# Kernel tuning notes

Measured on AMD Instinct MI355X. Metric: run time of the kernel, lower is better.

## Reference

```python
import jax, jax.numpy as jnp
import numpy as np
import math

L, H, NH, NKV, HD = 18, 1024, 8, 1, 256
FF, HOR, PRE, B, AD = 4096, 50, 968, 8, 32
EPS = 1e-6
NEG = -1e9
SCALE = HD ** -0.5


def setup_inputs() -> dict:
    key = jax.random.key(0)
    ks = iter(jax.random.split(key, 64))
    n = lambda shape, s=0.02: jax.random.normal(next(ks), shape, jnp.float32) * s
    return {
        'prefix_keys':    jax.random.normal(next(ks), (B, L, NKV, PRE, HD), jnp.float32),
        'prefix_values':  jax.random.normal(next(ks), (B, L, NKV, PRE, HD), jnp.float32),
        'x_t':            jax.random.normal(next(ks), (B, HOR, AD), jnp.float32),
        'timestep':       jax.random.uniform(next(ks), (B,), jnp.float32),
        'prefix_pad_masks': jnp.ones((B, PRE), jnp.bool_),
        'action_in_w': n((AD, H)), 'action_in_b': jnp.zeros((H,), jnp.float32),
        'action_out_w': n((H, AD)), 'action_out_b': jnp.zeros((AD,), jnp.float32),
        'tmlp_in_w': n((H, H)), 'tmlp_in_b': jnp.zeros((H,), jnp.float32),
        'tmlp_out_w': n((H, H)), 'tmlp_out_b': jnp.zeros((H,), jnp.float32),
        'w_q': n((L, H, NH * HD)), 'w_k': n((L, H, NKV * HD)), 'w_v': n((L, H, NKV * HD)),
        'w_o': n((L, NH * HD, H)),
        'w_gate': n((L, H, FF)), 'w_up': n((L, H, FF)), 'w_down': n((L, FF, H)),
        'in_norm_w': jnp.zeros((L, H), jnp.float32), 'in_scale_w': n((L, H, H)), 'in_gate_w': n((L, H, H)),
        'post_norm_w': jnp.zeros((L, H), jnp.float32), 'post_scale_w': n((L, H, H)), 'post_gate_w': n((L, H, H)),
        'fnorm_w': jnp.zeros((H,), jnp.float32), 'fnorm_scale_w': n((H, H)),
    }


def _rmsnorm(x, w):
    v = jnp.mean(x * x, axis=-1, keepdims=True)
    return x * jax.lax.rsqrt(v + EPS) * (1.0 + w)


def _ada_rmsnorm(x, w, cond, w_scale, w_gate):
    # AdaRMSNorm: rmsnorm scaled by (1 + dense(cond)); returns gate = dense(cond)
    normed = _rmsnorm(x, w)
    scale = cond @ w_scale                     # [B, H]
    gate = cond @ w_gate                       # [B, H]
    return normed * (1.0 + scale[:, None, :]), gate[:, None, :]


def _time_cond(timestep, tmlp_in_w, tmlp_in_b, tmlp_out_w, tmlp_out_b):
    half = H // 2
    frac = jnp.linspace(0.0, 1.0, half)
    period = 0.004 * (4.0 / 0.004) ** frac
    ang = (2.0 * math.pi / period)[None, :] * timestep[:, None]   # [B, half]
    emb = jnp.concatenate([jnp.sin(ang), jnp.cos(ang)], axis=1)   # [B, H]
    emb = jax.nn.silu(emb @ tmlp_in_w + tmlp_in_b)
    return jax.nn.silu(emb @ tmlp_out_w + tmlp_out_b)


def _rope(x, cos, sin):
    x1, x2 = jnp.split(x, 2, axis=-1)
    return x * cos + jnp.concatenate([-x2, x1], axis=-1) * sin


def _attn(q, k, v, mask):
    # q: [B,NH,S,D], k/v: [B,NKV,T,D]; GQA via grouped einsum (no KV materialized expansion)
    G = NH // NKV
    qg = q.reshape(B, NKV, G, HOR, HD)
    s = jnp.einsum('bkgsd,bktd->bkgst', qg, k) * SCALE + mask
    p = jax.nn.softmax(s.astype(jnp.float32), axis=-1).astype(q.dtype)
    return jnp.einsum('bkgst,bktd->bkgsd', p, v).reshape(B, NH, HOR, HD)


def _forward(prefix_pad_masks, prefix_keys, prefix_values, x_t, timestep,
             action_in_w, action_in_b, action_out_w, action_out_b,
             tmlp_in_w, tmlp_in_b, tmlp_out_w, tmlp_out_b,
             w_q, w_k, w_v, w_o, w_gate, w_up, w_down,
             in_norm_w, in_scale_w, in_gate_w,
             post_norm_w, post_scale_w, post_gate_w,
             fnorm_w, fnorm_scale_w):
    cond = _time_cond(timestep, tmlp_in_w, tmlp_in_b, tmlp_out_w, tmlp_out_b)  # [B,H]
    h = x_t @ action_in_w + action_in_b                                        # [B,HOR,H]

    # prefix-bidirectional + causal-suffix mask: [HOR, PRE+HOR]
    mask = jnp.zeros((HOR, PRE + HOR), jnp.float32)
    mask = mask.at[:, PRE:].set(jnp.triu(jnp.full((HOR, HOR), NEG, jnp.float32), k=1))

    # rotary at suffix positions = prefix valid count + arange(HOR)
    offsets = jnp.sum(prefix_pad_masks.astype(jnp.int32), axis=-1, keepdims=True)
    pos = (offsets + jnp.arange(HOR)[None, :]).astype(jnp.float32)             # [B,HOR]
    inv_freq = 1.0 / (10000.0 ** (jnp.arange(0, HD, 2).astype(jnp.float32) / HD))
    ang = pos[:, :, None] * inv_freq[None, None, :]                            # [B,HOR,HD/2]
    cos = jnp.concatenate([jnp.cos(ang), jnp.cos(ang)], axis=-1)[:, None]      # [B,1,HOR,HD]
    sin = jnp.concatenate([jnp.sin(ang), jnp.sin(ang)], axis=-1)[:, None]

    for i in range(L):
        normed, gate = _ada_rmsnorm(h, in_norm_w[i], cond, in_scale_w[i], in_gate_w[i])
        q = (normed @ w_q[i]).reshape(B, HOR, NH, HD).transpose(0, 2, 1, 3)
        k = (normed @ w_k[i]).reshape(B, HOR, NKV, HD).transpose(0, 2, 1, 3)
        v = (normed @ w_v[i]).reshape(B, HOR, NKV, HD).transpose(0, 2, 1, 3)
        q = _rope(q, cos, sin)
        k = _rope(k, cos, sin)
        fk = jnp.concatenate([prefix_keys[:, i], k], axis=2)                    # [B,NKV,PRE+HOR,HD]
        fv = jnp.concatenate([prefix_values[:, i], v], axis=2)
        att = _attn(q, fk, fv, mask)
        att = att.transpose(0, 2, 1, 3).reshape(B, HOR, NH * HD)
        h1 = h + gate * (att @ w_o[i])                                          # gated residual
        normed2, gate2 = _ada_rmsnorm(h1, post_norm_w[i], cond, post_scale_w[i], post_gate_w[i])
        mlp = (jax.nn.gelu(normed2 @ w_gate[i]) * (normed2 @ w_up[i])) @ w_down[i]
        h = h1 + gate2 * mlp

    scale = cond @ fnorm_scale_w
    h = _rmsnorm(h, fnorm_w) * (1.0 + scale[:, None, :])
    return h @ action_out_w + action_out_b


def reference(prefix_keys, prefix_values, x_t, timestep, prefix_pad_masks,
              action_in_w, action_in_b, action_out_w, action_out_b,
              tmlp_in_w, tmlp_in_b, tmlp_out_w, tmlp_out_b,
              w_q, w_k, w_v, w_o, w_gate, w_up, w_down,
              in_norm_w, in_scale_w, in_gate_w,
              post_norm_w, post_scale_w, post_gate_w,
              fnorm_w, fnorm_scale_w):
    return _forward(prefix_pad_masks, prefix_keys, prefix_values, x_t, timestep,
                    action_in_w, action_in_b, action_out_w, action_out_b,
                    tmlp_in_w, tmlp_in_b, tmlp_out_w, tmlp_out_b,
                    w_q, w_k, w_v, w_o, w_gate, w_up, w_down,
                    in_norm_w, in_scale_w, in_gate_w,
                    post_norm_w, post_scale_w, post_gate_w,
                    fnorm_w, fnorm_scale_w)
```

## Files before the change

### kernel.cpp

```cpp
#include <hip/hip_runtime.h>

#define L_ 18
#define H_ 1024
#define NH_ 8
#define HD_ 256
#define FF_ 4096
#define HOR_ 50
#define PRE_ 968
#define B_ 8
#define AD_ 32
#define TPAD_ 1024
#define MROWS_ 400
#define MPAD_ 512
#define KSTEP_ 128
#define LST_ 132

typedef float f32x4 __attribute__((ext_vector_type(4)));
typedef short s16x4 __attribute__((ext_vector_type(4)));
typedef short s16x8 __attribute__((ext_vector_type(8)));
typedef unsigned short u16x8 __attribute__((ext_vector_type(8)));

__device__ __forceinline__ unsigned short f2bf(float f) {
  unsigned u = __float_as_uint(f);
  u += 0x7FFFu + ((u >> 16) & 1u);
  return (unsigned short)(u >> 16);
}
__device__ __forceinline__ float bf2f(unsigned short h) {
  return __uint_as_float(((unsigned)h) << 16);
}
__device__ __forceinline__ float wave_sum(float v) {
#pragma unroll
  for (int o = 32; o > 0; o >>= 1) v += __shfl_xor(v, o);
  return v;
}

__global__ __launch_bounds__(256) void emb_k(const float* __restrict__ ts, float* __restrict__ emb) {
  int b = blockIdx.x, tid = threadIdx.x;
  float t = ts[b];
  for (int j = tid; j < 512; j += 256) {
    float ang = 1570.7963267948966f * expf((float)j * (-6.907755278982137f / 511.0f)) * t;
    emb[(size_t)b * H_ + j] = sinf(ang);
    emb[(size_t)b * H_ + 512 + j] = cosf(ang);
  }
}

__global__ __launch_bounds__(256) void gemm8_k(const float* __restrict__ A8, const float* __restrict__ W,
                                               const float* __restrict__ bias, float* __restrict__ out,
                                               int act) {
  __shared__ float a_s[8 * 1024];
  __shared__ float red[4][8][64];
  int tid = threadIdx.x;
  for (int i = tid; i < 8 * 1024; i += 256) a_s[i] = A8[i];
  __syncthreads();
  int nl = tid & 63, kg = tid >> 6;
  int n = blockIdx.x * 64 + nl;
  float acc[8];
#pragma unroll
  for (int m = 0; m < 8; m++) acc[m] = 0.f;
  for (int k = kg * 256; k < kg * 256 + 256; k++) {
    float wv = W[(size_t)k * 1024 + n];
#pragma unroll
    for (int m = 0; m < 8; m++) acc[m] += a_s[m * 1024 + k] * wv;
  }
#pragma unroll
  for (int m = 0; m < 8; m++) red[kg][m][nl] = acc[m];
  __syncthreads();
  if (kg == 0) {
#pragma unroll
    for (int m = 0; m < 8; m++) {
      float v = red[0][m][nl] + red[1][m][nl] + red[2][m][nl] + red[3][m][nl];
      if (bias) v += bias[n];
      if (act) v = v / (1.f + expf(-v));
      out[(size_t)m * 1024 + n] = v;
    }
  }
}

__global__ __launch_bounds__(256) void gates_k(const float* __restrict__ cond,
                                               const float* __restrict__ w0, const float* __restrict__ w1,
                                               const float* __restrict__ w2, const float* __restrict__ w3,
                                               float* __restrict__ gates) {
  __shared__ float a_s[8 * 1024];
  __shared__ float red[4][8][64];
  int tid = threadIdx.x;
  for (int i = tid; i < 8 * 1024; i += 256) a_s[i] = cond[i];
  __syncthreads();
  int z = blockIdx.z, layer = blockIdx.y;
  const float* W = (z == 0 ? w0 : z == 1 ? w1 : z == 2 ? w2 : w3) + (size_t)layer * H_ * H_;
  float* out = gates + ((size_t)(z * L_ + layer) * 8) * H_;
  int nl = tid & 63, kg = tid >> 6;
  int n = blockIdx.x * 64 + nl;
  float acc[8];
#pragma unroll
  for (int m = 0; m < 8; m++) acc[m] = 0.f;
  for (int k = kg * 256; k < kg * 256 + 256; k++) {
    float wv = W[(size_t)k * 1024 + n];
#pragma unroll
    for (int m = 0; m < 8; m++) acc[m] += a_s[m * 1024 + k] * wv;
  }
#pragma unroll
  for (int m = 0; m < 8; m++) red[kg][m][nl] = acc[m];
  __syncthreads();
  if (kg == 0) {
#pragma unroll
    for (int m = 0; m < 8; m++)
      out[(size_t)m * 1024 + n] = red[0][m][nl] + red[1][m][nl] + red[2][m][nl] + red[3][m][nl];
  }
}

__global__ void offs_k(const unsigned char* __restrict__ mask, int* __restrict__ offs) {
  __shared__ int cnt[8];
  __shared__ int mod4;
  int tid = threadIdx.x;
  if (tid < 8) cnt[tid] = 0;
  if (tid == 8) mod4 = 0;
  __syncthreads();
  for (int i = tid; i < B_ * PRE_; i += 256) {
    unsigned char v = mask[i];
    if (v) {
      atomicAdd(&cnt[i / PRE_], 1);
      if (i & 3) atomicAdd(&mod4, 1);
    }
  }
  __syncthreads();
  if (tid < 8) offs[tid] = (mod4 == 0) ? cnt[tid] * 4 : cnt[tid];
}

__global__ __launch_bounds__(256) void action_in_k(const float* __restrict__ xt, const float* __restrict__ Wi,
                                                   const float* __restrict__ bi, float* __restrict__ h) {
  int idx = blockIdx.x * 256 + threadIdx.x;
  int m = idx >> 10, n = idx & 1023;
  float v = 0.f;
  if (m < MROWS_) {
    const float* xr = xt + (size_t)m * AD_;
#pragma unroll
    for (int k = 0; k < AD_; k++) v += xr[k] * Wi[(size_t)k * H_ + n];
    v += bi[n];
  }
  h[idx] = v;
}

__global__ __launch_bounds__(256) void ada_k(const float* __restrict__ X, const float* __restrict__ nw,
                                             const float* __restrict__ sc, unsigned short* __restrict__ Y) {
  int m = blockIdx.x, tid = threadIdx.x;
  size_t base = (size_t)m * H_;
  if (m >= MROWS_) {
#pragma unroll
    for (int j = 0; j < 4; j++) Y[base + tid * 4 + j] = 0;
    return;
  }
  f32x4 x = *(const f32x4*)(X + base + tid * 4);
  float ss = x[0] * x[0] + x[1] * x[1] + x[2] * x[2] + x[3] * x[3];
  __shared__ float r4[4];
  float wsv = wave_sum(ss);
  if ((tid & 63) == 0) r4[tid >> 6] = wsv;
  __syncthreads();
  float rs = rsqrtf((r4[0] + r4[1] + r4[2] + r4[3]) * (1.f / 1024.f) + 1e-6f);
  int b = m / HOR_;
#pragma unroll
  for (int j = 0; j < 4; j++) {
    int n = tid * 4 + j;
    Y[base + n] = f2bf(x[j] * rs * (1.f + nw[n]) * (1.f + sc[(size_t)b * H_ + n]));
  }
}

__global__ __launch_bounds__(256) void prefixAll_k(const float* __restrict__ pk, const float* __restrict__ pv,
                                                   unsigned short* __restrict__ Kf_all,
                                                   unsigned short* __restrict__ Vt_all) {
  int b = blockIdx.y, t0 = blockIdx.x * 64, layer = blockIdx.z, tid = threadIdx.x;
  unsigned short* Kf = Kf_all + (size_t)layer * B_ * TPAD_ * HD_;
  unsigned short* Vt = Vt_all + (size_t)layer * B_ * HD_ * TPAD_;
  __shared__ unsigned short vt[256][72];
  const float* kp = pk + ((size_t)(b * L_ + layer)) * PRE_ * HD_;
  const float* vp = pv + ((size_t)(b * L_ + layer)) * PRE_ * HD_;
  for (int i = 0; i < 64; i++) {
    int t = t0 + i;
    float kv = 0.f, vv = 0.f;
    if (t < PRE_) {
      kv = kp[(size_t)t * HD_ + tid];
      vv = vp[(size_t)t * HD_ + tid];
    }
    Kf[((size_t)b * TPAD_ + t) * HD_ + tid] = f2bf(kv);
    vt[tid][i] = f2bf(vv);
  }
  __syncthreads();
#pragma unroll
  for (int p = 0; p < 4; p++) {
    int d = p * 64 + (tid >> 2);
    int c0 = (tid & 3) * 16;
    u16x8 v0, v1;
#pragma unroll
    for (int j = 0; j < 8; j++) { v0[j] = vt[d][c0 + j]; v1[j] = vt[d][c0 + 8 + j]; }
    size_t dst = ((size_t)(b * HD_ + d)) * TPAD_ + t0 + c0;
    *(u16x8*)(Vt + dst) = v0;
    *(u16x8*)(Vt + dst + 8) = v1;
  }
}

__global__ __launch_bounds__(512) void qkvF_k(const unsigned short* __restrict__ A,
                                              const float* __restrict__ Wq, const float* __restrict__ Wk,
                                              const float* __restrict__ Wv, const int* __restrict__ offs,
                                              unsigned short* __restrict__ q_r, unsigned short* __restrict__ Kf,
                                              unsigned short* __restrict__ Vt) {
  const int st = blockIdx.x, mh = blockIdx.y;
  const int tid = threadIdx.x, wv = tid >> 6, l = tid & 63;
  const int lr = l & 15, kg = l >> 4, lk = kg << 2;
  const int m0 = mh * 256 + wv * 32;

  const float* W;
  int ldw, wbase;
  bool paired;
  if (st < 64)      { W = Wq; ldw = 2048; wbase = (st >> 3) * 256 + (st & 7) * 16; paired = true; }
  else if (st < 72) { W = Wk; ldw = 256;  wbase = (st - 64) * 16; paired = true; }
  else              { W = Wv; ldw = 256;  wbase = (st - 72) * 32; paired = false; }

  __shared__ unsigned short Wt[2][32][LST_];
  __shared__ int offsL[8];
  const int pr = tid >> 3, c0 = (tid & 7) * 4;
  const int wcol = wbase + c0 + ((paired && c0 >= 16) ? 112 : 0);

  if (tid < 8) offsL[tid] = offs[tid];

  f32x4 acc[2][2];
#pragma unroll
  for (int a = 0; a < 2; a++)
#pragma unroll
    for (int b = 0; b < 2; b++) acc[a][b] = (f32x4){0.f, 0.f, 0.f, 0.f};

  f32x4 pa0, pa1;
  auto LOADW = [&](int IT) {
    size_t kk = (size_t)IT * KSTEP_ + 2 * pr;
    pa0 = *(const f32x4*)(W + kk * ldw + wcol);
    pa1 = *(const f32x4*)(W + (kk + 1) * ldw + wcol);
  };
  auto STOREW = [&](int BUF) {
#pragma unroll
    for (int j = 0; j < 4; j++) {
      unsigned v = (unsigned)f2bf(pa0[j]) | ((unsigned)f2bf(pa1[j]) << 16);
      *(unsigned*)&Wt[BUF][c0 + j][2 * pr] = v;
    }
  };

  LOADW(0);
  STOREW(0);
  __syncthreads();

  for (int it = 0; it < 8; ++it) {
    if (it + 1 < 8) LOADW(it + 1);
    const int cur = it & 1, kb = it * KSTEP_;
#pragma unroll
    for (int s = 0; s < 4; s++) {
      s16x8 bfr[2];
#pragma unroll
      for (int nf = 0; nf < 2; nf++) {
        const unsigned short* wp = &Wt[cur][nf * 16 + lr][s * 32 + 2 * lk];
        s16x4 b0 = *(const s16x4*)wp;
        s16x4 b1 = *(const s16x4*)(wp + 4);
#pragma unroll
        for (int j = 0; j < 4; j++) { bfr[nf][j] = b0[j]; bfr[nf][4 + j] = b1[j]; }
      }
#pragma unroll
      for (int mf = 0; mf < 2; mf++) {
        s16x8 a = *(const s16x8*)(A + (size_t)(m0 + mf * 16 + lr) * H_ + kb + s * 32 + 8 * kg);
#pragma unroll
        for (int nf = 0; nf < 2; nf++)
          acc[mf][nf] = __builtin_amdgcn_mfma_f32_16x16x32_bf16(a, bfr[nf], acc[mf][nf], 0, 0, 0);
      }
    }
    if (it + 1 < 8) STOREW((it + 1) & 1);
    __syncthreads();
  }

  const float RK = -9.210340371976184f / 128.0f;
  if (st < 64) {
    const int h = st >> 3, x = (st & 7) * 16, dd = x + lr;
    const float inv = expf((float)dd * RK);
#pragma unroll
    for (int mf = 0; mf < 2; mf++)
#pragma unroll
      for (int r = 0; r < 4; r++) {
        int m = m0 + mf * 16 + lk + r;
        if (m >= MROWS_) continue;
        int b = m / HOR_, s = m - b * HOR_;
        float ang = (float)(offsL[b] + s) * inv;
        float cc = cosf(ang), sn = sinf(ang);
        float v1 = acc[mf][0][r], v2 = acc[mf][1][r];
        size_t base = ((size_t)(b * NH_ + h) * 64 + s) * HD_;
        q_r[base + dd] = f2bf(v1 * cc - v2 * sn);
        q_r[base + dd + 128] = f2bf(v2 * cc + v1 * sn);
      }
  } else if (st < 72) {
    const int x = (st - 64) * 16, dd = x + lr;
    const float inv = expf((float)dd * RK);
#pragma unroll
    for (int mf = 0; mf < 2; mf++)
#pragma unroll
      for (int r = 0; r < 4; r++) {
        int m = m0 + mf * 16 + lk + r;
        if (m >= MROWS_) continue;
        int b = m / HOR_, s = m - b * HOR_;
        float ang = (float)(offsL[b] + s) * inv;
        float cc = cosf(ang), sn = sinf(ang);
        float v1 = acc[mf][0][r], v2 = acc[mf][1][r];
        size_t base = ((size_t)b * TPAD_ + PRE_ + s) * HD_;
        Kf[base + dd] = f2bf(v1 * cc - v2 * sn);
        Kf[base + dd + 128] = f2bf(v2 * cc + v1 * sn);
      }
  } else {
    const int x = (st - 72) * 32;
#pragma unroll
    for (int mf = 0; mf < 2; mf++)
#pragma unroll
      for (int nf = 0; nf < 2; nf++)
#pragma unroll
        for (int r = 0; r < 4; r++) {
          int m = m0 + mf * 16 + lk + r;
          if (m >= MROWS_) continue;
          int b = m / HOR_, s = m - b * HOR_;
          int d = x + nf * 16 + lr;
          Vt[((size_t)(b * HD_ + d)) * TPAD_ + PRE_ + s] = f2bf(acc[mf][nf][r]);
        }
  }
}

__global__ __launch_bounds__(512) void flash8_k(const unsigned short* __restrict__ qr,
                                                const unsigned short* __restrict__ Kf,
                                                const unsigned short* __restrict__ Vt,
                                                unsigned short* __restrict__ attb) {
  const int b = blockIdx.x, rg = blockIdx.y, h = blockIdx.z;
  const int bh = b * NH_ + h;
  const int tid = threadIdx.x, w = tid >> 6, l = tid & 63;
  const int lr = l & 15, kg = l >> 4;
  const int t0 = w * 128;

  __shared__ __align__(16) unsigned short Pl[8][16][136];
  __shared__ float mlS[8][16][2];

  const unsigned short* qbase = qr + ((size_t)bh * 64 + rg * 16 + lr) * HD_;
  s16x8 afr[8];
#pragma unroll
  for (int js = 0; js < 8; js++) afr[js] = *(const s16x8*)(qbase + js * 32 + 8 * kg);
  f32x4 sc[8];
#pragma unroll
  for (int nf = 0; nf < 8; nf++) sc[nf] = (f32x4){0.f, 0.f, 0.f, 0.f};
  const unsigned short* kb = Kf + ((size_t)b * TPAD_ + t0) * HD_;
#pragma unroll
  for (int js = 0; js < 8; js++)
#pragma unroll
    for (int nf = 0; nf < 8; nf++) {
      s16x8 bv = *(const s16x8*)(kb + (size_t)(nf * 16 + lr) * HD_ + js * 32 + 8 * kg);
      sc[nf] = __builtin_amdgcn_mfma_f32_16x16x32_bf16(afr[js], bv, sc[nf], 0, 0, 0);
    }
  float mx[4] = {-3.0e38f, -3.0e38f, -3.0e38f, -3.0e38f};
#pragma unroll
  for (int nf = 0; nf < 8; nf++) {
    int t = t0 + nf * 16 + lr;
#pragma unroll
    for (int r = 0; r < 4; r++) {
      int srw = rg * 16 + 4 * kg + r;
      float v = sc[nf][r] * 0.0625f;
      if (t >= PRE_ && (t - PRE_) > srw) v = -1e9f;
      sc[nf][r] = v;
      mx[r] = fmaxf(mx[r], v);
    }
  }
#pragma unroll
  for (int o = 8; o > 0; o >>= 1)
#pragma unroll
    for (int r = 0; r < 4; r++) mx[r] = fmaxf(mx[r], __shfl_xor(mx[r], o));
  float ls[4] = {0.f, 0.f, 0.f, 0.f};
#pragma unroll
  for (int nf = 0; nf < 8; nf++)
#pragma unroll
    for (int r = 0; r < 4; r++) {
      float p = expf(sc[nf][r] - mx[r]);
      sc[nf][r] = p;
      ls[r] += p;
    }
#pragma unroll
  for (int o = 8; o > 0; o >>= 1)
#pragma unroll
    for (int r = 0; r < 4; r++) ls[r] += __shfl_xor(ls[r], o);
#pragma unroll
  for (int nf = 0; nf < 8; nf++)
#pragma unroll
    for (int r = 0; r < 4; r++) Pl[w][4 * kg + r][nf * 16 + lr] = f2bf(sc[nf][r]);
  if (lr == 0) {
#pragma unroll
    for (int r = 0; r < 4; r++) {
      mlS[w][4 * kg + r][0] = mx[r];
      mlS[w][4 * kg + r][1] = ls[r];
    }
  }
  __syncthreads();
  f32x4 o4[8][2];
#pragma unroll
  for (int a = 0; a < 8; a++)
#pragma unroll
    for (int c = 0; c < 2; c++) o4[a][c] = (f32x4){0.f, 0.f, 0.f, 0.f};
#pragma unroll
  for (int wz = 0; wz < 8; wz++)
#pragma unroll
    for (int ti = 0; ti < 128; ti += 32) {
      s16x8 a = *(const s16x8*)&Pl[wz][lr][ti + 8 * kg];
#pragma unroll
      for (int nf = 0; nf < 2; nf++) {
        s16x8 bv = *(const s16x8*)(Vt + ((size_t)(b * HD_ + w * 32 + nf * 16 + lr)) * TPAD_ +
                                   wz * 128 + ti + 8 * kg);
        o4[wz][nf] = __builtin_amdgcn_mfma_f32_16x16x32_bf16(a, bv, o4[wz][nf], 0, 0, 0);
      }
    }
#pragma unroll
  for (int r = 0; r < 4; r++) {
    int row = 4 * kg + r;
    int s = rg * 16 + row;
    if (s >= HOR_) continue;
    float M = -3.0e38f;
#pragma unroll
    for (int wz = 0; wz < 8; wz++) M = fmaxf(M, mlS[wz][row][0]);
    float w8[8], Lden = 0.f;
#pragma unroll
    for (int wz = 0; wz < 8; wz++) {
      w8[wz] = expf(mlS[wz][row][0] - M);
      Lden += w8[wz] * mlS[wz][row][1];
    }
    float invL = 1.f / Lden;
#pragma unroll
    for (int nf = 0; nf < 2; nf++) {
      float o = 0.f;
#pragma unroll
      for (int wz = 0; wz < 8; wz++) o += w8[wz] * o4[wz][nf][r];
      attb[((size_t)(b * HOR_ + s)) * 2048 + h * HD_ + w * 32 + nf * 16 + lr] = f2bf(o * invL);
    }
  }
}

template <int MODE, int NS, int MS>
__global__ __launch_bounds__(512) void gemmS_k(const unsigned short* __restrict__ A, int lda, int Ksz,
                                               const float* __restrict__ W0, const float* __restrict__ W1,
                                               float* __restrict__ part, unsigned short* __restrict__ outT) {
  constexpr int NCOL = (MODE == 2) ? 64 : 32;
  constexpr int NF = NCOL / 16;
  constexpr int RPW = 64 / MS;
  constexpr int MFC = RPW / 16;
  const int tid = threadIdx.x;
  const int wv = tid >> 6, l = tid & 63;
  const int lr = l & 15, lk = (l >> 4) << 2;
  const int n0 = blockIdx.x * 32;
  const int kz = blockIdx.y;
  const int KC = Ksz / NS;
  const int kbase = kz * KC;
  const int m0 = (int)blockIdx.z * (512 / MS) + wv * RPW;

  const float* Wg = W0;
  const float* Wu = W1;
  const int ldw = (MODE == 2) ? 4096 : 1024;

  __shared__ unsigned short Wt[2][NCOL][LST_];
  const int pr = tid >> 3;
  const int c0 = (tid & 7) * 4;

  f32x4 acc[MFC][NF];
#pragma unroll
  for (int a = 0; a < MFC; a++)
#pragma unroll
    for (int b = 0; b < NF; b++) acc[a][b] = (f32x4){0.f, 0.f, 0.f, 0.f};

  const int niter = KC / KSTEP_;
  f32x4 pa0, pa1, pb0, pb1;

  auto LOADW = [&](int IT) {
    size_t kk = (size_t)(kbase + IT * KSTEP_ + 2 * pr);
    pa0 = *(const f32x4*)(Wg + kk * ldw + n0 + c0);
    pa1 = *(const f32x4*)(Wg + (kk + 1) * ldw + n0 + c0);
    if (MODE == 2) {
      pb0 = *(const f32x4*)(Wu + kk * ldw + n0 + c0);
      pb1 = *(const f32x4*)(Wu + (kk + 1) * ldw + n0 + c0);
    }
  };
  auto STOREW = [&](int BUF) {
#pragma unroll
    for (int j = 0; j < 4; j++) {
      unsigned v = (unsigned)f2bf(pa0[j]) | ((unsigned)f2bf(pa1[j]) << 16);
      *(unsigned*)&Wt[BUF][c0 + j][2 * pr] = v;
      if (MODE == 2) {
        unsigned u = (unsigned)f2bf(pb0[j]) | ((unsigned)f2bf(pb1[j]) << 16);
        *(unsigned*)&Wt[BUF][32 + c0 + j][2 * pr] = u;
      }
    }
  };

  LOADW(0);
  STOREW(0);
  __syncthreads();

  for (int it = 0; it < niter; ++it) {
    if (it + 1 < niter) LOADW(it + 1);
    const int cur = it & 1;
    const int kb = kbase + it * KSTEP_;
#pragma unroll
    for (int s = 0; s < 4; s++) {
      s16x8 bfr[NF];
#pragma unroll
      for (int nf = 0; nf < NF; nf++) {
        const unsigned short* wp = &Wt[cur][nf * 16 + lr][s * 32 + 2 * lk];
        s16x4 b0 = *(const s16x4*)wp;
        s16x4 b1 = *(const s16x4*)(wp + 4);
#pragma unroll
        for (int j = 0; j < 4; j++) { bfr[nf][j] = b0[j]; bfr[nf][4 + j] = b1[j]; }
      }
#pragma unroll
      for (int mf = 0; mf < MFC; mf++) {
        s16x8 a = *(const s16x8*)(A + (size_t)(m0 + mf * 16 + lr) * lda + kb + s * 32 + 2 * lk);
#pragma unroll
        for (int nf = 0; nf < NF; nf++)
          acc[mf][nf] = __builtin_amdgcn_mfma_f32_16x16x32_bf16(a, bfr[nf], acc[mf][nf], 0, 0, 0);
      }
    }
    if (it + 1 < niter) STOREW((it + 1) & 1);
    __syncthreads();
  }

  if (MODE == 2) {
#pragma unroll
    for (int mf = 0; mf < MFC; mf++)
#pragma unroll
      for (int nf = 0; nf < 2; nf++)
#pragma unroll
        for (int r = 0; r < 4; r++) {
          int row = m0 + mf * 16 + lk + r;
          if (row >= MROWS_) continue;
          int col = n0 + nf * 16 + lr;
          float g = acc[mf][nf][r];
          float u = acc[mf][nf + 2][r];
          g = 0.5f * g * (1.f + tanhf(0.7978845608028654f * (g + 0.044715f * g * g * g)));
          outT[(size_t)row * 4096 + col] = f2bf(g * u);
        }
  } else {
#pragma unroll
    for (int mf = 0; mf < MFC; mf++)
#pragma unroll
      for (int nf = 0; nf < NF; nf++)
#pragma unroll
        for (int r = 0; r < 4; r++) {
          int row = m0 + mf * 16 + lk + r;
          if (row >= MROWS_) continue;
          int col = n0 + nf * 16 + lr;
          part[((size_t)kz * MPAD_ + row) * 1024 + col] = acc[mf][nf][r];
        }
  }
}

template <int NS>
__global__ __launch_bounds__(256) void redA_k(const float* __restrict__ part, const float* __restrict__ prev,
                                              const float* __restrict__ gatev, const float* __restrict__ nw,
                                              const float* __restrict__ sc, float* __restrict__ outH,
                                              unsigned short* __restrict__ outN) {
  int r = blockIdx.x, tid = threadIdx.x;
  int c = tid * 4;
  f32x4 h = (f32x4){0.f, 0.f, 0.f, 0.f};
  int b = 0;
  if (r < MROWS_) {
    b = r / HOR_;
    f32x4 v = (f32x4){0.f, 0.f, 0.f, 0.f};
#pragma unroll
    for (int z = 0; z < NS; z++) v += *(const f32x4*)(part + ((size_t)z * MPAD_ + r) * H_ + c);
    f32x4 pv = *(const f32x4*)(prev + (size_t)r * H_ + c);
    f32x4 gv = *(const f32x4*)(gatev + (size_t)b * H_ + c);
    h = pv + gv * v;
  }
  *(f32x4*)(outH + (size_t)r * H_ + c) = h;
  float ss = h[0] * h[0] + h[1] * h[1] + h[2] * h[2] + h[3] * h[3];
  __shared__ float r4[4];
  float wsv = wave_sum(ss);
  if ((tid & 63) == 0) r4[tid >> 6] = wsv;
  __syncthreads();
  float rs = rsqrtf((r4[0] + r4[1] + r4[2] + r4[3]) * (1.f / 1024.f) + 1e-6f);
#pragma unroll
  for (int j = 0; j < 4; j++) {
    int n = c + j;
    outN[(size_t)r * H_ + n] = f2bf(h[j] * rs * (1.f + nw[n]) * (1.f + sc[(size_t)b * H_ + n]));
  }
}

__global__ __launch_bounds__(256) void fout_k(const unsigned short* __restrict__ nf, const float* __restrict__ Wo,
                                              const float* __restrict__ bo, float* __restrict__ out) {
  int m = blockIdx.x, tid = threadIdx.x;
  int n = tid & 31, kg = tid >> 5;
  float acc = 0.f;
  for (int k = kg * 128; k < kg * 128 + 128; k++)
    acc += bf2f(nf[(size_t)m * H_ + k]) * Wo[(size_t)k * AD_ + n];
  __shared__ float red[8][32];
  red[kg][n] = acc;
  __syncthreads();
  if (kg == 0) {
    float v = 0.f;
#pragma unroll
    for (int g = 0; g < 8; g++) v += red[g][n];
    out[(size_t)m * AD_ + n] = v + bo[n];
  }
}

extern "C" void kernel_launch(void* const* d_in, const int* in_sizes, int n_in,
                              void* d_out, int out_size, void* d_ws, size_t ws_size,
                              hipStream_t stream) {
  const float* prefix_keys   = (const float*)d_in[0];
  const float* prefix_values = (const float*)d_in[1];
  const float* x_t           = (const float*)d_in[2];
  const float* timestep      = (const float*)d_in[3];
  const unsigned char* pad_mask = (const unsigned char*)d_in[4];
  const float* action_in_w   = (const float*)d_in[5];
  const float* action_in_b   = (const float*)d_in[6];
  const float* action_out_w  = (const float*)d_in[7];
  const float* action_out_b  = (const float*)d_in[8];
  const float* tmlp_in_w     = (const float*)d_in[9];
  const float* tmlp_in_b     = (const float*)d_in[10];
  const float* tmlp_out_w    = (const float*)d_in[11];
  const float* tmlp_out_b    = (const float*)d_in[12];
  const float* w_q    = (const float*)d_in[13];
  const float* w_k    = (const float*)d_in[14];
  const float* w_v    = (const float*)d_in[15];
  const float* w_o    = (const float*)d_in[16];
  const float* w_gate = (const float*)d_in[17];
  const float* w_up   = (const float*)d_in[18];
  const float* w_down = (const float*)d_in[19];
  const float* in_norm_w    = (const float*)d_in[20];
  const float* in_scale_w   = (const float*)d_in[21];
  const float* in_gate_w    = (const float*)d_in[22];
  const float* post_norm_w  = (const float*)d_in[23];
  const float* post_scale_w = (const float*)d_in[24];
  const float* post_gate_w  = (const float*)d_in[25];
  const float* fnorm_w       = (const float*)d_in[26];
  const float* fnorm_scale_w = (const float*)d_in[27];

  char* wsp = (char*)d_ws;
  auto alloc = [&](size_t bytes) { void* p = (void*)wsp; wsp += (bytes + 255) & ~(size_t)255; return p; };

  float* emb0   = (float*)alloc((size_t)8 * H_ * 4);
  float* emb1   = (float*)alloc((size_t)8 * H_ * 4);
  float* cond   = (float*)alloc((size_t)8 * H_ * 4);
  float* fscale = (float*)alloc((size_t)8 * H_ * 4);
  float* gates  = (float*)alloc((size_t)4 * L_ * 8 * H_ * 4);
  int*   offs   = (int*)alloc(64);
  float* hbuf   = (float*)alloc((size_t)MPAD_ * H_ * 4);
  float* h1buf  = (float*)alloc((size_t)MPAD_ * H_ * 4);
  unsigned short* normed  = (unsigned short*)alloc((size_t)MPAD_ * H_ * 2);
  unsigned short* normed2 = (unsigned short*)alloc((size_t)MPAD_ * H_ * 2);
  unsigned short* q_r     = (unsigned short*)alloc((size_t)B_ * NH_ * 64 * HD_ * 2);
  unsigned short* Kf_all  = (unsigned short*)alloc((size_t)L_ * B_ * TPAD_ * HD_ * 2);
  unsigned short* Vt_all  = (unsigned short*)alloc((size_t)L_ * B_ * HD_ * TPAD_ * 2);
  unsigned short* attb    = (unsigned short*)alloc((size_t)MPAD_ * 2048 * 2);
  unsigned short* t_buf   = (unsigned short*)alloc((size_t)MPAD_ * FF_ * 2);
  float* wopart = (float*)alloc((size_t)4 * MPAD_ * 1024 * 4);
  float* dpart  = (float*)alloc((size_t)4 * MPAD_ * 1024 * 4);

  hipMemsetAsync(attb + (size_t)MROWS_ * 2048, 0, (size_t)(MPAD_ - MROWS_) * 2048 * 2, stream);

  emb_k<<<8, 256, 0, stream>>>(timestep, emb0);
  gemm8_k<<<16, 256, 0, stream>>>(emb0, tmlp_in_w, tmlp_in_b, emb1, 1);
  gemm8_k<<<16, 256, 0, stream>>>(emb1, tmlp_out_w, tmlp_out_b, cond, 1);
  gemm8_k<<<16, 256, 0, stream>>>(cond, fnorm_scale_w, nullptr, fscale, 0);
  gates_k<<<dim3(16, L_, 4), 256, 0, stream>>>(cond, in_scale_w, in_gate_w, post_scale_w, post_gate_w, gates);
  offs_k<<<1, 256, 0, stream>>>(pad_mask, offs);
  action_in_k<<<(MPAD_ * H_) / 256, 256, 0, stream>>>(x_t, action_in_w, action_in_b, hbuf);
  prefixAll_k<<<dim3(16, B_, L_), 256, 0, stream>>>(prefix_keys, prefix_values, Kf_all, Vt_all);
  ada_k<<<MPAD_, 256, 0, stream>>>(hbuf, in_norm_w, gates, normed);

  for (int i = 0; i < L_; i++) {
    const float* wq_i = w_q + (size_t)i * H_ * 2048;
    const float* wk_i = w_k + (size_t)i * H_ * HD_;
    const float* wv_i = w_v + (size_t)i * H_ * HD_;
    const float* wo_i = w_o + (size_t)i * 2048 * H_;
    const float* wg_i = w_gate + (size_t)i * H_ * FF_;
    const float* wu_i = w_up + (size_t)i * H_ * FF_;
    const float* wd_i = w_down + (size_t)i * FF_ * H_;
    const float* g_in_gate    = gates + ((size_t)(1 * L_ + i) * 8) * H_;
    const float* g_post_scale = gates + ((size_t)(2 * L_ + i) * 8) * H_;
    const float* g_post_gate  = gates + ((size_t)(3 * L_ + i) * 8) * H_;
    unsigned short* Kf_l = Kf_all + (size_t)i * B_ * TPAD_ * HD_;
    unsigned short* Vt_l = Vt_all + (size_t)i * B_ * HD_ * TPAD_;

    qkvF_k<<<dim3(80, 2), 512, 0, stream>>>(normed, wq_i, wk_i, wv_i, offs, q_r, Kf_l, Vt_l);
    flash8_k<<<dim3(B_, 4, NH_), 512, 0, stream>>>(q_r, Kf_l, Vt_l, attb);
    gemmS_k<1, 4, 2><<<dim3(32, 4, 2), 512, 0, stream>>>(attb, 2048, 2048, wo_i, nullptr, wopart, nullptr);
    redA_k<4><<<MPAD_, 256, 0, stream>>>(wopart, hbuf, g_in_gate, post_norm_w + (size_t)i * H_,
                                         g_post_scale, h1buf, normed2);
    gemmS_k<2, 1, 2><<<dim3(128, 1, 2), 512, 0, stream>>>(normed2, H_, H_, wg_i, wu_i, nullptr, t_buf);
    gemmS_k<3, 4, 2><<<dim3(32, 4, 2), 512, 0, stream>>>(t_buf, FF_, FF_, wd_i, nullptr, dpart, nullptr);
    const float* nw_next = (i + 1 < L_) ? in_norm_w + (size_t)(i + 1) * H_ : fnorm_w;
    const float* sc_next = (i + 1 < L_) ? gates + ((size_t)(i + 1) * 8) * H_ : fscale;
    redA_k<4><<<MPAD_, 256, 0, stream>>>(dpart, h1buf, g_post_gate, nw_next, sc_next, hbuf, normed);
  }

  fout_k<<<MROWS_, 256, 0, stream>>>(normed, action_out_w, action_out_b, (float*)d_out);
}
```

Measured before the change: 2.945 ms.

## Prefetch A fragments into registers, add dedicated gate/up kernel, trim pad rows

The activation (A) fragments for the next K-step are now loaded into registers during the current step, in both the QKV kernel and the generic split GEMM, so global-load latency overlaps with MFMA work. The gate/up projection moves to a new upg_k kernel that covers 256 rows per block over 2 row-halves, replacing the split-K gemmS_k MODE 2 launch. The residual/norm reduction kernels now launch only over the 400 real rows, and the padded rows of normed2 and t_buf are zeroed once up front. The cost is more register pressure from the prefetch buffers, which may lower occupancy.

New measurement: 2.665 ms. 1.1x faster.

```diff
diff --git a/kernel.cpp b/kernel.cpp
--- a/kernel.cpp
+++ b/kernel.cpp
@@ -241,13 +241,24 @@
     }
   };
 
+  s16x8 aP[2][4];
+  auto LOADA = [&](int IT) {
+    const int kb = IT * KSTEP_;
+#pragma unroll
+    for (int s = 0; s < 4; s++)
+#pragma unroll
+      for (int mf = 0; mf < 2; mf++)
+        aP[mf][s] = *(const s16x8*)(A + (size_t)(m0 + mf * 16 + lr) * H_ + kb + s * 32 + 8 * kg);
+  };
+
   LOADW(0);
+  LOADA(0);
   STOREW(0);
   __syncthreads();
 
   for (int it = 0; it < 8; ++it) {
     if (it + 1 < 8) LOADW(it + 1);
-    const int cur = it & 1, kb = it * KSTEP_;
+    const int cur = it & 1;
 #pragma unroll
     for (int s = 0; s < 4; s++) {
       s16x8 bfr[2];
@@ -260,14 +271,15 @@
         for (int j = 0; j < 4; j++) { bfr[nf][j] = b0[j]; bfr[nf][4 + j] = b1[j]; }
       }
 #pragma unroll
-      for (int mf = 0; mf < 2; mf++) {
-        s16x8 a = *(const s16x8*)(A + (size_t)(m0 + mf * 16 + lr) * H_ + kb + s * 32 + 8 * kg);
+      for (int mf = 0; mf < 2; mf++)
 #pragma unroll
         for (int nf = 0; nf < 2; nf++)
-          acc[mf][nf] = __builtin_amdgcn_mfma_f32_16x16x32_bf16(a, bfr[nf], acc[mf][nf], 0, 0, 0);
-      }
-    }
-    if (it + 1 < 8) STOREW((it + 1) & 1);
+          acc[mf][nf] = __builtin_amdgcn_mfma_f32_16x16x32_bf16(aP[mf][s], bfr[nf], acc[mf][nf], 0, 0, 0);
+    }
+    if (it + 1 < 8) {
+      LOADA(it + 1);
+      STOREW((it + 1) & 1);
+    }
     __syncthreads();
   }
 
@@ -490,14 +502,24 @@
     }
   };
 
+  s16x8 aP[MFC][4];
+  auto LOADA = [&](int IT) {
+    const int kb = kbase + IT * KSTEP_;
+#pragma unroll
+    for (int s = 0; s < 4; s++)
+#pragma unroll
+      for (int mf = 0; mf < MFC; mf++)
+        aP[mf][s] = *(const s16x8*)(A + (size_t)(m0 + mf * 16 + lr) * lda + kb + s * 32 + 2 * lk);
+  };
+
   LOADW(0);
+  LOADA(0);
   STOREW(0);
   __syncthreads();
 
   for (int it = 0; it < niter; ++it) {
     if (it + 1 < niter) LOADW(it + 1);
     const int cur = it & 1;
-    const int kb = kbase + it * KSTEP_;
 #pragma unroll
     for (int s = 0; s < 4; s++) {
       s16x8 bfr[NF];
@@ -510,14 +532,15 @@
         for (int j = 0; j < 4; j++) { bfr[nf][j] = b0[j]; bfr[nf][4 + j] = b1[j]; }
       }
 #pragma unroll
-      for (int mf = 0; mf < MFC; mf++) {
-        s16x8 a = *(const s16x8*)(A + (size_t)(m0 + mf * 16 + lr) * lda + kb + s * 32 + 2 * lk);
+      for (int mf = 0; mf < MFC; mf++)
 #pragma unroll
         for (int nf = 0; nf < NF; nf++)
-          acc[mf][nf] = __builtin_amdgcn_mfma_f32_16x16x32_bf16(a, bfr[nf], acc[mf][nf], 0, 0, 0);
-      }
-    }
-    if (it + 1 < niter) STOREW((it + 1) & 1);
+          acc[mf][nf] = __builtin_amdgcn_mfma_f32_16x16x32_bf16(aP[mf][s], bfr[nf], acc[mf][nf], 0, 0, 0);
+    }
+    if (it + 1 < niter) {
+      LOADA(it + 1);
+      STOREW((it + 1) & 1);
+    }
     __syncthreads();
   }
 
@@ -558,17 +581,13 @@
                                               unsigned short* __restrict__ outN) {
   int r = blockIdx.x, tid = threadIdx.x;
   int c = tid * 4;
-  f32x4 h = (f32x4){0.f, 0.f, 0.f, 0.f};
-  int b = 0;
-  if (r < MROWS_) {
-    b = r / HOR_;
-    f32x4 v = (f32x4){0.f, 0.f, 0.f, 0.f};
-#pragma unroll
-    for (int z = 0; z < NS; z++) v += *(const f32x4*)(part + ((size_t)z * MPAD_ + r) * H_ + c);
-    f32x4 pv = *(const f32x4*)(prev + (size_t)r * H_ + c);
-    f32x4 gv = *(const f32x4*)(gatev + (size_t)b * H_ + c);
-    h = pv + gv * v;
-  }
+  int b = r / HOR_;
+  f32x4 v = (f32x4){0.f, 0.f, 0.f, 0.f};
+#pragma unroll
+  for (int z = 0; z < NS; z++) v += *(const f32x4*)(part + ((size_t)z * MPAD_ + r) * H_ + c);
+  f32x4 pv = *(const f32x4*)(prev + (size_t)r * H_ + c);
+  f32x4 gv = *(const f32x4*)(gatev + (size_t)b * H_ + c);
+  f32x4 h = pv + gv * v;
   *(f32x4*)(outH + (size_t)r * H_ + c) = h;
   float ss = h[0] * h[0] + h[1] * h[1] + h[2] * h[2] + h[3] * h[3];
   __shared__ float r4[4];
@@ -581,6 +600,99 @@
     int n = c + j;
     outN[(size_t)r * H_ + n] = f2bf(h[j] * rs * (1.f + nw[n]) * (1.f + sc[(size_t)b * H_ + n]));
   }
+}
+
+__global__ __launch_bounds__(512) void upg_k(const unsigned short* __restrict__ A, const float* __restrict__ Wg,
+                                             const float* __restrict__ Wu, unsigned short* __restrict__ tb) {
+  const int st = blockIdx.x, mh = blockIdx.y;
+  const int n0 = st * 32;
+  const int tid = threadIdx.x, wv = tid >> 6, l = tid & 63;
+  const int lr = l & 15, kg = l >> 4, lk = kg << 2;
+  const int m0 = mh * 256 + wv * 32;
+
+  __shared__ unsigned short Wt[2][64][LST_];
+  const int pr = tid >> 3, c0 = (tid & 7) * 4;
+
+  f32x4 acc[2][4];
+#pragma unroll
+  for (int a = 0; a < 2; a++)
+#pragma unroll
+    for (int b = 0; b < 4; b++) acc[a][b] = (f32x4){0.f, 0.f, 0.f, 0.f};
+
+  f32x4 pa0, pa1, pb0, pb1;
+  auto LOADW = [&](int IT) {
+    size_t kk = (size_t)IT * KSTEP_ + 2 * pr;
+    pa0 = *(const f32x4*)(Wg + kk * 4096 + n0 + c0);
+    pa1 = *(const f32x4*)(Wg + (kk + 1) * 4096 + n0 + c0);
+    pb0 = *(const f32x4*)(Wu + kk * 4096 + n0 + c0);
+    pb1 = *(const f32x4*)(Wu + (kk + 1) * 4096 + n0 + c0);
+  };
+  auto STOREW = [&](int BUF) {
+#pragma unroll
+    for (int j = 0; j < 4; j++) {
+      unsigned v = (unsigned)f2bf(pa0[j]) | ((unsigned)f2bf(pa1[j]) << 16);
+      *(unsigned*)&Wt[BUF][c0 + j][2 * pr] = v;
+      unsigned u = (unsigned)f2bf(pb0[j]) | ((unsigned)f2bf(pb1[j]) << 16);
+      *(unsigned*)&Wt[BUF][32 + c0 + j][2 * pr] = u;
+    }
+  };
+
+  s16x8 aP[2][4];
+  auto LOADA = [&](int IT) {
+    const int kb = IT * KSTEP_;
+#pragma unroll
+    for (int s = 0; s < 4; s++)
+#pragma unroll
+      for (int mf = 0; mf < 2; mf++)
+        aP[mf][s] = *(const s16x8*)(A + (size_t)(m0 + mf * 16 + lr) * H_ + kb + s * 32 + 8 * kg);
+  };
+
+  LOADW(0);
+  LOADA(0);
+  STOREW(0);
+  __syncthreads();
+
+  for (int it = 0; it < 8; ++it) {
+    if (it + 1 < 8) LOADW(it + 1);
+    const int cur = it & 1;
+#pragma unroll
+    for (int s = 0; s < 4; s++) {
+      s16x8 bfr[4];
+#pragma unroll
+      for (int nf = 0; nf < 4; nf++) {
+        const unsigned short* wp = &Wt[cur][nf * 16 + lr][s * 32 + 2 * lk];
+        s16x4 b0 = *(const s16x4*)wp;
+        s16x4 b1 = *(const s16x4*)(wp + 4);
+#pragma unroll
+        for (int j = 0; j < 4; j++) { bfr[nf][j] = b0[j]; bfr[nf][4 + j] = b1[j]; }
+      }
+#pragma unroll
+      for (int mf = 0; mf < 2; mf++)
+#pragma unroll
+        for (int nf = 0; nf < 4; nf++)
+          acc[mf][nf] = __builtin_amdgcn_mfma_f32_16x16x32_bf16(aP[mf][s], bfr[nf], acc[mf][nf], 0, 0, 0);
+    }
+    if (it + 1 < 8) {
+      LOADA(it + 1);
+      STOREW((it + 1) & 1);
+    }
+    __syncthreads();
+  }
+
+#pragma unroll
+  for (int mf = 0; mf < 2; mf++)
+#pragma unroll
+    for (int nf = 0; nf < 2; nf++)
+#pragma unroll
+      for (int r = 0; r < 4; r++) {
+        int row = m0 + mf * 16 + lk + r;
+        if (row >= MROWS_) continue;
+        int col = n0 + nf * 16 + lr;
+        float g = acc[mf][nf][r];
+        float u = acc[mf][nf + 2][r];
+        g = 0.5f * g * (1.f + tanhf(0.7978845608028654f * (g + 0.044715f * g * g * g)));
+        tb[(size_t)row * 4096 + col] = f2bf(g * u);
+      }
 }
 
 __global__ __launch_bounds__(256) void fout_k(const unsigned short* __restrict__ nf, const float* __restrict__ Wo,
@@ -655,6 +767,8 @@
   float* dpart  = (float*)alloc((size_t)4 * MPAD_ * 1024 * 4);
 
   hipMemsetAsync(attb + (size_t)MROWS_ * 2048, 0, (size_t)(MPAD_ - MROWS_) * 2048 * 2, stream);
+  hipMemsetAsync(normed2 + (size_t)MROWS_ * H_, 0, (size_t)(MPAD_ - MROWS_) * H_ * 2, stream);
+  hipMemsetAsync(t_buf + (size_t)MROWS_ * FF_, 0, (size_t)(MPAD_ - MROWS_) * FF_ * 2, stream);
 
   emb_k<<<8, 256, 0, stream>>>(timestep, emb0);
   gemm8_k<<<16, 256, 0, stream>>>(emb0, tmlp_in_w, tmlp_in_b, emb1, 1);
@@ -683,13 +797,13 @@
     qkvF_k<<<dim3(80, 2), 512, 0, stream>>>(normed, wq_i, wk_i, wv_i, offs, q_r, Kf_l, Vt_l);
     flash8_k<<<dim3(B_, 4, NH_), 512, 0, stream>>>(q_r, Kf_l, Vt_l, attb);
     gemmS_k<1, 4, 2><<<dim3(32, 4, 2), 512, 0, stream>>>(attb, 2048, 2048, wo_i, nullptr, wopart, nullptr);
-    redA_k<4><<<MPAD_, 256, 0, stream>>>(wopart, hbuf, g_in_gate, post_norm_w + (size_t)i * H_,
-                                         g_post_scale, h1buf, normed2);
-    gemmS_k<2, 1, 2><<<dim3(128, 1, 2), 512, 0, stream>>>(normed2, H_, H_, wg_i, wu_i, nullptr, t_buf);
+    redA_k<4><<<MROWS_, 256, 0, stream>>>(wopart, hbuf, g_in_gate, post_norm_w + (size_t)i * H_,
+                                          g_post_scale, h1buf, normed2);
+    upg_k<<<dim3(128, 2), 512, 0, stream>>>(normed2, wg_i, wu_i, t_buf);
     gemmS_k<3, 4, 2><<<dim3(32, 4, 2), 512, 0, stream>>>(t_buf, FF_, FF_, wd_i, nullptr, dpart, nullptr);
     const float* nw_next = (i + 1 < L_) ? in_norm_w + (size_t)(i + 1) * H_ : fnorm_w;
     const float* sc_next = (i + 1 < L_) ? gates + ((size_t)(i + 1) * 8) * H_ : fscale;
-    redA_k<4><<<MPAD_, 256, 0, stream>>>(dpart, h1buf, g_post_gate, nw_next, sc_next, hbuf, normed);
+    redA_k<4><<<MROWS_, 256, 0, stream>>>(dpart, h1buf, g_post_gate, nw_next, sc_next, hbuf, normed);
   }
 
   fout_k<<<MROWS_, 256, 0, stream>>>(normed, action_out_w, action_out_b, (float*)d_out);
```
